# Performance work log

Measured on AMD Instinct MI355X. Metric: run time of the kernel, lower is better.

Reference implementation:

```python
import jax, jax.numpy as jnp
import numpy as np

NUM_EMBEDDINGS = 512
EMBEDDING_DIM = 64
COMMITMENT_COST = 0.25
N = 262144


def setup_inputs() -> dict:
    key = jax.random.key(0)
    k1, k2 = jax.random.split(key)
    inputs = jax.random.normal(k1, (N, EMBEDDING_DIM), dtype=jnp.float32)
    # torch init: uniform(-1/num_embeddings, 1/num_embeddings)
    emb_weight = jax.random.uniform(
        k2, (NUM_EMBEDDINGS, EMBEDDING_DIM), dtype=jnp.float32,
        minval=-1.0 / NUM_EMBEDDINGS, maxval=1.0 / NUM_EMBEDDINGS)
    return {"inputs": inputs, "emb_weight": emb_weight}


def reference(inputs, emb_weight):
    # squared L2 distances to every codebook entry: [N, K]
    distances = (jnp.sum(inputs ** 2, axis=1, keepdims=True)
                 + jnp.sum(emb_weight ** 2, axis=1)
                 - 2.0 * inputs @ emb_weight.T)
    encoding_indices = jnp.argmin(distances, axis=1)          # [N]
    quantized = emb_weight[encoding_indices]                  # direct gather == onehot @ W

    e_latent_loss = jnp.mean((jax.lax.stop_gradient(quantized) - inputs) ** 2)
    q_latent_loss = jnp.mean((quantized - jax.lax.stop_gradient(inputs)) ** 2)
    loss = q_latent_loss + COMMITMENT_COST * e_latent_loss

    # straight-through estimator
    quantized_st = inputs + jax.lax.stop_gradient(quantized - inputs)

    # avg_probs = mean over rows of the one-hot encodings -> normalized histogram
    counts = jnp.zeros((NUM_EMBEDDINGS,), dtype=jnp.float32).at[encoding_indices].add(1.0)
    avg_probs = counts / inputs.shape[0]
    perplexity = jnp.exp(-jnp.sum(avg_probs * jnp.log(avg_probs + 1e-10)))
    norm_perplexity = perplexity / NUM_EMBEDDINGS

    return (loss, quantized_st, norm_perplexity, encoding_indices[:, None])
```

## Files before the change

### kernel.cpp

```cpp
#include <hip/hip_runtime.h>

#define N_ROWS 262144
#define DIM 64
#define KCODES 512
#define THREADS 512
#define BLK_ROWS 128
#define NBLOCKS (N_ROWS / BLK_ROWS)
#define CHUNK 128
#define NCHUNK (KCODES / CHUNK)
#define NPART 64
#define MARGIN_T 1.25e-4f

#define OFF_Q 1
#define OFF_PERP (1 + (size_t)N_ROWS * DIM)
#define OFF_IDX (2 + (size_t)N_ROWS * DIM)

typedef __attribute__((ext_vector_type(8))) short bf16x8;
typedef __attribute__((ext_vector_type(4))) float f32x4;


__device__ __forceinline__ float np_sum_sq64(const float* __restrict__ v) {
#pragma clang fp contract(off)
    float r[8];
#pragma unroll
    for (int l = 0; l < 8; ++l) r[l] = v[l] * v[l];
#pragma unroll
    for (int k = 1; k < 8; ++k) {
#pragma unroll
        for (int l = 0; l < 8; ++l) {
            float sq = v[8 * k + l] * v[8 * k + l];
            r[l] = r[l] + sq;
        }
    }
    return ((r[0] + r[1]) + (r[2] + r[3])) + ((r[4] + r[5]) + (r[6] + r[7]));
}

__device__ __forceinline__ unsigned short f2bf(float f) {
    unsigned u = __float_as_uint(f);
    u += 0x7FFFu + ((u >> 16) & 1u);
    return (unsigned short)(u >> 16);
}
__device__ __forceinline__ float bf2f(unsigned short h) {
    return __uint_as_float((unsigned)h << 16);
}

__device__ __forceinline__ unsigned t2key(float t, unsigned idx) {
    return (__float_as_uint(t + 0.5f) & 0xFFFFFE00u) | idx;
}
__device__ __forceinline__ float key2t(unsigned key) {
    return __uint_as_float(key & 0xFFFFFE00u) - 0.5f;
}


__global__ __launch_bounds__(256) void vq_prep(const float* __restrict__ W,
        unsigned short* __restrict__ WhiG, unsigned short* __restrict__ WloG,
        float* __restrict__ Bsc) {
    int c = blockIdx.x * 256 + threadIdx.x;
    if (c >= KCODES) return;
    const float* w = W + (size_t)c * DIM;
    Bsc[c] = np_sum_sq64(w);
#pragma unroll 4
    for (int d = 0; d < DIM; ++d) {
        float v = -2.0f * w[d];
        unsigned short hi = f2bf(v);
        unsigned short lo = f2bf(v - bf2f(hi));
        WhiG[c * DIM + d] = hi;
        WloG[c * DIM + d] = lo;
    }
}


__global__ __launch_bounds__(THREADS, 4) void vq_argmin(
    const float* __restrict__ X,
    const unsigned short* __restrict__ WhiG,
    const unsigned short* __restrict__ WloG,
    const float* __restrict__ Bsc,
    float* __restrict__ out,
    double* __restrict__ sseAcc,
    unsigned* __restrict__ gHistP,
    int* __restrict__ flagList,
    unsigned* __restrict__ gCnt) {

    __shared__ __align__(16) unsigned short sHi[CHUNK * DIM];
    __shared__ __align__(16) unsigned short sLo[CHUNK * DIM];
    __shared__ __align__(16) float sX[BLK_ROWS * DIM];
    __shared__ __align__(16) float sB[KCODES];
    __shared__ unsigned sHist[KCODES];
    __shared__ int sFlagRows[BLK_ROWS];
    __shared__ unsigned sCnt, sBase;
    __shared__ double sSseW[8];

    const int tid = threadIdx.x;
    const int w = tid >> 6;
    const int l = tid & 63;
    const int q = l >> 4;
    const int r16 = l & 15;
    const int R0 = blockIdx.x * BLK_ROWS;

    {
        const float4* g = (const float4*)(X + (size_t)R0 * DIM);
        char* base = (char*)sX;
#pragma unroll
        for (int i = 0; i < (BLK_ROWS * DIM / 4) / THREADS; ++i) {
            int fidx = tid + THREADS * i;
            int r = fidx >> 4, c4 = fidx & 15;
            int off = (r * 256 + c4 * 16) ^ ((r & 7) << 5);
            *(float4*)(base + off) = g[fidx];
        }
        sB[tid] = Bsc[tid];
        sHist[tid] = 0u;
        if (tid == 0) sCnt = 0u;
    }
    __syncthreads();

    bf16x8 xh[2], xl[2];
    float asum = 0.f;
    {
        const int r = w * 16 + r16;
        const char* base = (const char*)sX;
#pragma unroll
        for (int h = 0; h < 2; ++h) {
            int b0 = (r * 256 + h * 128 + q * 32) ^ ((r & 7) << 5);
            float4 fa = *(const float4*)(base + b0);
            float4 fb = *(const float4*)(base + b0 + 16);
            float f[8] = {fa.x, fa.y, fa.z, fa.w, fb.x, fb.y, fb.z, fb.w};
            bf16x8 hi8, lo8;
#pragma unroll
            for (int j = 0; j < 8; ++j) {
                asum = fmaf(f[j], f[j], asum);
                unsigned short hi = f2bf(f[j]);
                unsigned short lo = f2bf(f[j] - bf2f(hi));
                hi8[j] = (short)hi; lo8[j] = (short)lo;
            }
            xh[h] = hi8; xl[h] = lo8;
        }
    }

    unsigned min1 = 0xFFFFFFFFu, min2 = 0xFFFFFFFFu;

    for (int cc = 0; cc < NCHUNK; ++cc) {
        const int c0 = cc * CHUNK;
        __syncthreads();
        {
            const uint4* gh = (const uint4*)(WhiG + (size_t)c0 * DIM);
            const uint4* gl = (const uint4*)(WloG + (size_t)c0 * DIM);
            char* bh = (char*)sHi; char* bl = (char*)sLo;
#pragma unroll
            for (int i = 0; i < (CHUNK * DIM / 8) / THREADS; ++i) {
                int idx = tid + THREADS * i;
                int c = idx >> 3, k8 = idx & 7;
                int off = (c * 128 + k8 * 16) ^ ((c & 7) << 4);
                *(uint4*)(bh + off) = gh[idx];
                *(uint4*)(bl + off) = gl[idx];
            }
        }
        __syncthreads();

#pragma unroll
        for (int ct = 0; ct < CHUNK / 16; ++ct) {
            const int cloc = ct * 16 + r16;
            const char* bh = (const char*)sHi;
            const char* bl = (const char*)sLo;
            const int sw = (cloc & 7) << 4;
            int o0 = (cloc * 128 + 16 * q) ^ sw;
            int o1 = (cloc * 128 + 64 + 16 * q) ^ sw;
            bf16x8 ah0 = *(const bf16x8*)(bh + o0);
            bf16x8 ah1 = *(const bf16x8*)(bh + o1);
            bf16x8 al0 = *(const bf16x8*)(bl + o0);
            bf16x8 al1 = *(const bf16x8*)(bl + o1);

            f32x4 acc = *(const f32x4*)&sB[c0 + ct * 16 + q * 4];

            acc = __builtin_amdgcn_mfma_f32_16x16x32_bf16(ah0, xh[0], acc, 0, 0, 0);
            acc = __builtin_amdgcn_mfma_f32_16x16x32_bf16(ah1, xh[1], acc, 0, 0, 0);
            acc = __builtin_amdgcn_mfma_f32_16x16x32_bf16(ah0, xl[0], acc, 0, 0, 0);
            acc = __builtin_amdgcn_mfma_f32_16x16x32_bf16(ah1, xl[1], acc, 0, 0, 0);
            acc = __builtin_amdgcn_mfma_f32_16x16x32_bf16(al0, xh[0], acc, 0, 0, 0);
            acc = __builtin_amdgcn_mfma_f32_16x16x32_bf16(al1, xh[1], acc, 0, 0, 0);

            const unsigned jbase = (unsigned)(c0 + ct * 16 + q * 4);
            unsigned k0 = t2key(acc[0], jbase + 0u);
            unsigned k1 = t2key(acc[1], jbase + 1u);
            unsigned k2 = t2key(acc[2], jbase + 2u);
            unsigned k3 = t2key(acc[3], jbase + 3u);
            unsigned lo01 = k0 < k1 ? k0 : k1, hi01 = k0 < k1 ? k1 : k0;
            unsigned lo23 = k2 < k3 ? k2 : k3, hi23 = k2 < k3 ? k3 : k2;
            unsigned m1 = lo01 < lo23 ? lo01 : lo23;
            unsigned mm = lo01 < lo23 ? lo23 : lo01;
            unsigned hh = hi01 < hi23 ? hi01 : hi23;
            unsigned m2 = hh < mm ? hh : mm;
            unsigned nm = min1 < m1 ? m1 : min1;
            min1 = min1 < m1 ? min1 : m1;
            unsigned sm = min2 < m2 ? min2 : m2;
            min2 = sm < nm ? sm : nm;
        }
    }

#pragma unroll
    for (int d = 16; d <= 32; d <<= 1) {
        unsigned o1 = (unsigned)__shfl_xor((int)min1, d, 64);
        unsigned o2 = (unsigned)__shfl_xor((int)min2, d, 64);
        asum += __shfl_xor(asum, d, 64);
        unsigned n1 = min1 < o1 ? min1 : o1;
        unsigned mx = min1 > o1 ? min1 : o1;
        unsigned mn = min2 < o2 ? min2 : o2;
        unsigned n2 = mx < mn ? mx : mn;
        min1 = n1; min2 = n2;
    }

    const unsigned best = min1 & 511u;
    const float t1 = key2t(min1), t2 = key2t(min2);
    const bool flagged = (t2 < t1 + MARGIN_T);

    float ssev = 0.f;
    if (q == 0) {
        const int row = R0 + w * 16 + r16;
        out[OFF_IDX + row] = (float)best;
        if (!flagged) {
            ssev = asum + t1;
            atomicAdd(&sHist[best], 1u);
        } else {
            unsigned s = atomicAdd(&sCnt, 1u);
            sFlagRows[s] = row;
        }
    }
#pragma unroll
    for (int off = 32; off; off >>= 1) ssev += __shfl_down(ssev, off);
    if (l == 0) sSseW[w] = (double)ssev;
    __syncthreads();

    if (tid == 0) sBase = atomicAdd(gCnt, sCnt);
    {
        unsigned c = sHist[tid];
        if (c) atomicAdd(&gHistP[(blockIdx.x & (NPART - 1)) * KCODES + tid], c);
    }
    __syncthreads();
    if (tid < (int)sCnt) flagList[sBase + tid] = sFlagRows[tid];
    if (tid == 0) {
        double s = 0.0;
#pragma unroll
        for (int i = 0; i < 8; ++i) s += sSseW[i];
        atomicAdd(sseAcc, s);
    }
}


__global__ __launch_bounds__(512, 2) void vq_fixup(
    const float* __restrict__ X, const float* __restrict__ W,
    const float* __restrict__ Bsc, float* __restrict__ out,
    double* __restrict__ sseP, unsigned* __restrict__ gHistP,
    const int* __restrict__ flagList, const unsigned* __restrict__ gCnt) {
    __shared__ unsigned long long sKeyW[8];
    const unsigned total = *gCnt;
    const int t = threadIdx.x;
    const int wv = t >> 6, l = t & 63;

    for (unsigned i = blockIdx.x; i < total; i += gridDim.x) {
        const int row = flagList[i];

        float xr[DIM];
        {
            const float4* Xr4 = (const float4*)(X + (size_t)row * DIM);
#pragma unroll
            for (int k4 = 0; k4 < 16; ++k4) {
                float4 v = Xr4[k4];
                xr[4 * k4 + 0] = v.x; xr[4 * k4 + 1] = v.y;
                xr[4 * k4 + 2] = v.z; xr[4 * k4 + 3] = v.w;
            }
        }
        const float A = np_sum_sq64(xr);

        double acc = 0.0;
        {
            const float4* wr = (const float4*)(W + (size_t)t * DIM);
#pragma unroll
            for (int k4 = 0; k4 < 16; ++k4) {
                float4 f = wr[k4];
                acc = fma((double)f.x, (double)xr[4 * k4 + 0], acc);
                acc = fma((double)f.y, (double)xr[4 * k4 + 1], acc);
                acc = fma((double)f.z, (double)xr[4 * k4 + 2], acc);
                acc = fma((double)f.w, (double)xr[4 * k4 + 3], acc);
            }
        }
        unsigned long long bk;
        {
#pragma clang fp contract(off)
            float C2 = (float)(2.0 * acc);
            float e = (A + Bsc[t]) - C2;
            int iu = __float_as_int(e);
            unsigned u = ((unsigned)iu) ^ (((unsigned)(iu >> 31)) | 0x80000000u);
            bk = ((unsigned long long)u << 32) | (unsigned)t;
        }
#pragma unroll
        for (int d = 1; d < 64; d <<= 1) {
            unsigned long long o =
                (unsigned long long)__shfl_xor((long long)bk, d, 64);
            bk = bk < o ? bk : o;
        }
        if (l == 0) sKeyW[wv] = bk;
        __syncthreads();
        if (t == 0) {
            unsigned long long b = sKeyW[0];
#pragma unroll
            for (int k = 1; k < 8; ++k) if (sKeyW[k] < b) b = sKeyW[k];
            unsigned bestc = (unsigned)(b & 511ULL);
            unsigned u = (unsigned)(b >> 32);
            unsigned fb = (u & 0x80000000u) ? (u & 0x7FFFFFFFu) : ~u;
            float ebest = __uint_as_float(fb);
            out[OFF_IDX + row] = (float)bestc;
            atomicAdd(&gHistP[(i & (NPART - 1)) * KCODES + bestc], 1u);
            atomicAdd(&sseP[i & (NPART - 1)], (double)ebest);
        }
        __syncthreads();
    }
}


__global__ __launch_bounds__(256) void vq_scatter(
    const float* __restrict__ W, float* __restrict__ out) {
    const int gid = blockIdx.x * 256 + threadIdx.x;
    const int row = gid >> 6;
    const int lane = gid & 63;
    int idx = (int)out[OFF_IDX + row];
    if ((unsigned)idx >= KCODES) idx = KCODES - 1;
    out[OFF_Q + (size_t)row * DIM + lane] = W[(size_t)idx * DIM + lane];
}


__global__ __launch_bounds__(512) void vq_finalize(
    const double* __restrict__ sseAcc, const double* __restrict__ sseP,
    const unsigned* __restrict__ gHistP, float* __restrict__ out) {
    __shared__ float partial[8];
    const int t = threadIdx.x;
    unsigned c = 0;
#pragma unroll 8
    for (int p = 0; p < NPART; ++p) c += gHistP[p * KCODES + t];
    float pf = (float)c * (1.0f / (float)N_ROWS);
    float v = pf * logf(pf + 1e-10f);
#pragma unroll
    for (int off = 32; off; off >>= 1) v += __shfl_down(v, off);
    if ((t & 63) == 0) partial[t >> 6] = v;
    __syncthreads();
    if (t == 0) {
        float s = 0.f;
#pragma unroll
        for (int i = 0; i < 8; ++i) s += partial[i];
        out[OFF_PERP] = expf(-s) * (1.0f / (float)KCODES);
        double s2 = sseAcc[0];
#pragma unroll
        for (int i = 0; i < NPART; ++i) s2 += sseP[i];
        out[0] = (float)(1.25 * s2 * (1.0 / ((double)N_ROWS * (double)DIM)));
    }
}

extern "C" void kernel_launch(void* const* d_in, const int* in_sizes, int n_in,
                              void* d_out, int out_size, void* d_ws, size_t ws_size,
                              hipStream_t stream) {
    const float* X = (const float*)d_in[0];
    const float* W = (const float*)d_in[1];
    float* out = (float*)d_out;
    double* sseAcc = (double*)d_ws;
    double* sseP = (double*)((char*)d_ws + 64);
    unsigned* gCnt = (unsigned*)((char*)d_ws + 64 + NPART * sizeof(double));

    size_t zb = 64 + NPART * sizeof(double) + 64;
    if (zb > ws_size) zb = ws_size;
    hipMemsetAsync(d_ws, 0, zb, stream);

    uintptr_t sbase = ((uintptr_t)(out + OFF_Q) + 15) & ~(uintptr_t)15;
    unsigned short* WhiG = (unsigned short*)sbase;
    unsigned short* WloG = WhiG + (size_t)KCODES * DIM;
    float* Bsc = (float*)(WloG + (size_t)KCODES * DIM);
    unsigned* gHistP = (unsigned*)(Bsc + KCODES);
    int* flagList = (int*)(gHistP + (size_t)NPART * KCODES);
    hipMemsetAsync(gHistP, 0, (size_t)NPART * KCODES * sizeof(unsigned), stream);

    vq_prep<<<2, 256, 0, stream>>>(W, WhiG, WloG, Bsc);
    vq_argmin<<<NBLOCKS, THREADS, 0, stream>>>(X, WhiG, WloG, Bsc, out,
                                               sseAcc, gHistP, flagList, gCnt);
    vq_fixup<<<NBLOCKS, 512, 0, stream>>>(X, W, Bsc, out, sseP, gHistP,
                                          flagList, gCnt);
    vq_finalize<<<1, 512, 0, stream>>>(sseAcc, sseP, gHistP, out);
    vq_scatter<<<(N_ROWS * DIM) / 256, 256, 0, stream>>>(W, out);
}
```

Measured before the change: 269.2 us.

## Process two 16-row tiles per wave to reuse codebook fragments and drop X staging

Doubles rows per block so each wave computes two 16-row tiles against every codebook fragment loaded from LDS. This halves codebook LDS traffic and chunk loads per row, and interleaves independent MFMA chains. Inputs are now read straight from global memory into registers instead of staged through swizzled LDS. The 0.5 key bias is folded into the shared norm table. In exchange it uses more registers and launches half as many blocks, which may hurt occupancy and tail balance.

```diff
diff --git a/kernel.cpp b/kernel.cpp
--- a/kernel.cpp
+++ b/kernel.cpp
@@ -4,7 +4,7 @@
 #define DIM 64
 #define KCODES 512
 #define THREADS 512
-#define BLK_ROWS 128
+#define BLK_ROWS 256
 #define NBLOCKS (N_ROWS / BLK_ROWS)
 #define CHUNK 128
 #define NCHUNK (KCODES / CHUNK)
@@ -44,8 +44,8 @@
     return __uint_as_float((unsigned)h << 16);
 }
 
-__device__ __forceinline__ unsigned t2key(float t, unsigned idx) {
-    return (__float_as_uint(t + 0.5f) & 0xFFFFFE00u) | idx;
+__device__ __forceinline__ unsigned t2key_biased(float tb, unsigned idx) {
+    return (__float_as_uint(tb) & 0xFFFFFE00u) | idx;
 }
 __device__ __forceinline__ float key2t(unsigned key) {
     return __uint_as_float(key & 0xFFFFFE00u) - 0.5f;
@@ -83,7 +83,6 @@
 
     __shared__ __align__(16) unsigned short sHi[CHUNK * DIM];
     __shared__ __align__(16) unsigned short sLo[CHUNK * DIM];
-    __shared__ __align__(16) float sX[BLK_ROWS * DIM];
     __shared__ __align__(16) float sB[KCODES];
     __shared__ unsigned sHist[KCODES];
     __shared__ int sFlagRows[BLK_ROWS];
@@ -97,46 +96,40 @@
     const int r16 = l & 15;
     const int R0 = blockIdx.x * BLK_ROWS;
 
+    sB[tid] = Bsc[tid] + 0.5f;
+    sHist[tid] = 0u;
+    if (tid == 0) sCnt = 0u;
+
+    bf16x8 xhA[2], xlA[2], xhB[2], xlB[2];
+    float asumA = 0.f, asumB = 0.f;
     {
-        const float4* g = (const float4*)(X + (size_t)R0 * DIM);
-        char* base = (char*)sX;
-#pragma unroll
-        for (int i = 0; i < (BLK_ROWS * DIM / 4) / THREADS; ++i) {
-            int fidx = tid + THREADS * i;
-            int r = fidx >> 4, c4 = fidx & 15;
-            int off = (r * 256 + c4 * 16) ^ ((r & 7) << 5);
-            *(float4*)(base + off) = g[fidx];
-        }
-        sB[tid] = Bsc[tid];
-        sHist[tid] = 0u;
-        if (tid == 0) sCnt = 0u;
-    }
-    __syncthreads();
-
-    bf16x8 xh[2], xl[2];
-    float asum = 0.f;
-    {
-        const int r = w * 16 + r16;
-        const char* base = (const char*)sX;
+        const float* xrA = X + (size_t)(R0 + w * 32 + r16) * DIM;
+        const float* xrB = xrA + 16 * DIM;
 #pragma unroll
         for (int h = 0; h < 2; ++h) {
-            int b0 = (r * 256 + h * 128 + q * 32) ^ ((r & 7) << 5);
-            float4 fa = *(const float4*)(base + b0);
-            float4 fb = *(const float4*)(base + b0 + 16);
-            float f[8] = {fa.x, fa.y, fa.z, fa.w, fb.x, fb.y, fb.z, fb.w};
-            bf16x8 hi8, lo8;
+            float4 fa = *(const float4*)(xrA + 32 * h + 8 * q);
+            float4 fb = *(const float4*)(xrA + 32 * h + 8 * q + 4);
+            float fA[8] = {fa.x, fa.y, fa.z, fa.w, fb.x, fb.y, fb.z, fb.w};
+            float4 ga = *(const float4*)(xrB + 32 * h + 8 * q);
+            float4 gb = *(const float4*)(xrB + 32 * h + 8 * q + 4);
+            float fB[8] = {ga.x, ga.y, ga.z, ga.w, gb.x, gb.y, gb.z, gb.w};
+            bf16x8 hiA, loA, hiB, loB;
 #pragma unroll
             for (int j = 0; j < 8; ++j) {
-                asum = fmaf(f[j], f[j], asum);
-                unsigned short hi = f2bf(f[j]);
-                unsigned short lo = f2bf(f[j] - bf2f(hi));
-                hi8[j] = (short)hi; lo8[j] = (short)lo;
-            }
-            xh[h] = hi8; xl[h] = lo8;
-        }
-    }
-
-    unsigned min1 = 0xFFFFFFFFu, min2 = 0xFFFFFFFFu;
+                asumA = fmaf(fA[j], fA[j], asumA);
+                unsigned short h1 = f2bf(fA[j]);
+                hiA[j] = (short)h1; loA[j] = (short)f2bf(fA[j] - bf2f(h1));
+                asumB = fmaf(fB[j], fB[j], asumB);
+                unsigned short h2 = f2bf(fB[j]);
+                hiB[j] = (short)h2; loB[j] = (short)f2bf(fB[j] - bf2f(h2));
+            }
+            xhA[h] = hiA; xlA[h] = loA;
+            xhB[h] = hiB; xlB[h] = loB;
+        }
+    }
+
+    unsigned min1A = 0xFFFFFFFFu, min2A = 0xFFFFFFFFu;
+    unsigned min1B = 0xFFFFFFFFu, min2B = 0xFFFFFFFFu;
 
     for (int cc = 0; cc < NCHUNK; ++cc) {
         const int c0 = cc * CHUNK;
@@ -169,60 +162,93 @@
             bf16x8 al0 = *(const bf16x8*)(bl + o0);
             bf16x8 al1 = *(const bf16x8*)(bl + o1);
 
-            f32x4 acc = *(const f32x4*)&sB[c0 + ct * 16 + q * 4];
-
-            acc = __builtin_amdgcn_mfma_f32_16x16x32_bf16(ah0, xh[0], acc, 0, 0, 0);
-            acc = __builtin_amdgcn_mfma_f32_16x16x32_bf16(ah1, xh[1], acc, 0, 0, 0);
-            acc = __builtin_amdgcn_mfma_f32_16x16x32_bf16(ah0, xl[0], acc, 0, 0, 0);
-            acc = __builtin_amdgcn_mfma_f32_16x16x32_bf16(ah1, xl[1], acc, 0, 0, 0);
-            acc = __builtin_amdgcn_mfma_f32_16x16x32_bf16(al0, xh[0], acc, 0, 0, 0);
-            acc = __builtin_amdgcn_mfma_f32_16x16x32_bf16(al1, xh[1], acc, 0, 0, 0);
+            f32x4 accA = *(const f32x4*)&sB[c0 + ct * 16 + q * 4];
+            f32x4 accB = accA;
+
+            accA = __builtin_amdgcn_mfma_f32_16x16x32_bf16(ah0, xhA[0], accA, 0, 0, 0);
+            accB = __builtin_amdgcn_mfma_f32_16x16x32_bf16(ah0, xhB[0], accB, 0, 0, 0);
+            accA = __builtin_amdgcn_mfma_f32_16x16x32_bf16(ah1, xhA[1], accA, 0, 0, 0);
+            accB = __builtin_amdgcn_mfma_f32_16x16x32_bf16(ah1, xhB[1], accB, 0, 0, 0);
+            accA = __builtin_amdgcn_mfma_f32_16x16x32_bf16(ah0, xlA[0], accA, 0, 0, 0);
+            accB = __builtin_amdgcn_mfma_f32_16x16x32_bf16(ah0, xlB[0], accB, 0, 0, 0);
+            accA = __builtin_amdgcn_mfma_f32_16x16x32_bf16(ah1, xlA[1], accA, 0, 0, 0);
+            accB = __builtin_amdgcn_mfma_f32_16x16x32_bf16(ah1, xlB[1], accB, 0, 0, 0);
+            accA = __builtin_amdgcn_mfma_f32_16x16x32_bf16(al0, xhA[0], accA, 0, 0, 0);
+            accB = __builtin_amdgcn_mfma_f32_16x16x32_bf16(al0, xhB[0], accB, 0, 0, 0);
+            accA = __builtin_amdgcn_mfma_f32_16x16x32_bf16(al1, xhA[1], accA, 0, 0, 0);
+            accB = __builtin_amdgcn_mfma_f32_16x16x32_bf16(al1, xhB[1], accB, 0, 0, 0);
 
             const unsigned jbase = (unsigned)(c0 + ct * 16 + q * 4);
-            unsigned k0 = t2key(acc[0], jbase + 0u);
-            unsigned k1 = t2key(acc[1], jbase + 1u);
-            unsigned k2 = t2key(acc[2], jbase + 2u);
-            unsigned k3 = t2key(acc[3], jbase + 3u);
-            unsigned lo01 = k0 < k1 ? k0 : k1, hi01 = k0 < k1 ? k1 : k0;
-            unsigned lo23 = k2 < k3 ? k2 : k3, hi23 = k2 < k3 ? k3 : k2;
-            unsigned m1 = lo01 < lo23 ? lo01 : lo23;
-            unsigned mm = lo01 < lo23 ? lo23 : lo01;
-            unsigned hh = hi01 < hi23 ? hi01 : hi23;
-            unsigned m2 = hh < mm ? hh : mm;
-            unsigned nm = min1 < m1 ? m1 : min1;
-            min1 = min1 < m1 ? min1 : m1;
-            unsigned sm = min2 < m2 ? min2 : m2;
-            min2 = sm < nm ? sm : nm;
+            {
+                unsigned k0 = t2key_biased(accA[0], jbase + 0u);
+                unsigned k1 = t2key_biased(accA[1], jbase + 1u);
+                unsigned k2 = t2key_biased(accA[2], jbase + 2u);
+                unsigned k3 = t2key_biased(accA[3], jbase + 3u);
+                unsigned lo01 = k0 < k1 ? k0 : k1, hi01 = k0 < k1 ? k1 : k0;
+                unsigned lo23 = k2 < k3 ? k2 : k3, hi23 = k2 < k3 ? k3 : k2;
+                unsigned m1 = lo01 < lo23 ? lo01 : lo23;
+                unsigned mm = lo01 < lo23 ? lo23 : lo01;
+                unsigned hh = hi01 < hi23 ? hi01 : hi23;
+                unsigned m2 = hh < mm ? hh : mm;
+                unsigned nm = min1A < m1 ? m1 : min1A;
+                min1A = min1A < m1 ? min1A : m1;
+                unsigned sm = min2A < m2 ? min2A : m2;
+                min2A = sm < nm ? sm : nm;
+            }
+            {
+                unsigned k0 = t2key_biased(accB[0], jbase + 0u);
+                unsigned k1 = t2key_biased(accB[1], jbase + 1u);
+                unsigned k2 = t2key_biased(accB[2], jbase + 2u);
+                unsigned k3 = t2key_biased(accB[3], jbase + 3u);
+                unsigned lo01 = k0 < k1 ? k0 : k1, hi01 = k0 < k1 ? k1 : k0;
+                unsigned lo23 = k2 < k3 ? k2 : k3, hi23 = k2 < k3 ? k3 : k2;
+                unsigned m1 = lo01 < lo23 ? lo01 : lo23;
+                unsigned mm = lo01 < lo23 ? lo23 : lo01;
+                unsigned hh = hi01 < hi23 ? hi01 : hi23;
+                unsigned m2 = hh < mm ? hh : mm;
+                unsigned nm = min1B < m1 ? m1 : min1B;
+                min1B = min1B < m1 ? min1B : m1;
+                unsigned sm = min2B < m2 ? min2B : m2;
+                min2B = sm < nm ? sm : nm;
+            }
         }
     }
 
 #pragma unroll
     for (int d = 16; d <= 32; d <<= 1) {
-        unsigned o1 = (unsigned)__shfl_xor((int)min1, d, 64);
-        unsigned o2 = (unsigned)__shfl_xor((int)min2, d, 64);
-        asum += __shfl_xor(asum, d, 64);
-        unsigned n1 = min1 < o1 ? min1 : o1;
-        unsigned mx = min1 > o1 ? min1 : o1;
-        unsigned mn = min2 < o2 ? min2 : o2;
-        unsigned n2 = mx < mn ? mx : mn;
-        min1 = n1; min2 = n2;
-    }
-
-    const unsigned best = min1 & 511u;
-    const float t1 = key2t(min1), t2 = key2t(min2);
-    const bool flagged = (t2 < t1 + MARGIN_T);
+        unsigned o1 = (unsigned)__shfl_xor((int)min1A, d, 64);
+        unsigned o2 = (unsigned)__shfl_xor((int)min2A, d, 64);
+        asumA += __shfl_xor(asumA, d, 64);
+        unsigned n1 = min1A < o1 ? min1A : o1;
+        unsigned mx = min1A > o1 ? min1A : o1;
+        unsigned mn = min2A < o2 ? min2A : o2;
+        min2A = mn < mx ? mn : mx; min1A = n1;
+
+        unsigned p1 = (unsigned)__shfl_xor((int)min1B, d, 64);
+        unsigned p2 = (unsigned)__shfl_xor((int)min2B, d, 64);
+        asumB += __shfl_xor(asumB, d, 64);
+        unsigned m1 = min1B < p1 ? min1B : p1;
+        unsigned my = min1B > p1 ? min1B : p1;
+        unsigned mz = min2B < p2 ? min2B : p2;
+        min2B = mz < my ? mz : my; min1B = m1;
+    }
 
     float ssev = 0.f;
     if (q == 0) {
-        const int row = R0 + w * 16 + r16;
-        out[OFF_IDX + row] = (float)best;
-        if (!flagged) {
-            ssev = asum + t1;
-            atomicAdd(&sHist[best], 1u);
-        } else {
-            unsigned s = atomicAdd(&sCnt, 1u);
-            sFlagRows[s] = row;
-        }
+        const int rowA = R0 + w * 32 + r16;
+        const int rowB = rowA + 16;
+        const unsigned bestA = min1A & 511u;
+        const unsigned bestB = min1B & 511u;
+        const float t1A = key2t(min1A), t2A = key2t(min2A);
+        const float t1B = key2t(min1B), t2B = key2t(min2B);
+        const bool flagA = (t2A < t1A + MARGIN_T);
+        const bool flagB = (t2B < t1B + MARGIN_T);
+        out[OFF_IDX + rowA] = (float)bestA;
+        out[OFF_IDX + rowB] = (float)bestB;
+        if (!flagA) { ssev += asumA + t1A; atomicAdd(&sHist[bestA], 1u); }
+        else { unsigned s = atomicAdd(&sCnt, 1u); sFlagRows[s] = rowA; }
+        if (!flagB) { ssev += asumB + t1B; atomicAdd(&sHist[bestB], 1u); }
+        else { unsigned s = atomicAdd(&sCnt, 1u); sFlagRows[s] = rowB; }
     }
 #pragma unroll
     for (int off = 32; off; off >>= 1) ssev += __shfl_down(ssev, off);
```

Measured after the change: 241.8 us. 1.11x faster.
